# Kernel tuning notes

Measured on AMD Instinct MI355X. Metric: run time of the kernel, lower is better.

## Reference

```python
import jax, jax.numpy as jnp
import numpy as np

N = 512   # state size
D = 512   # input/output feature size
L = 16384 # sequence length


def setup_inputs() -> dict:
    key = jax.random.key(0)
    kA, kB, kC, ku = jax.random.split(key, 4)
    # Scale/shift A so eigenvalues have negative real part (circular law radius 1,
    # shifted by -1.5) -> stable recurrence over L steps; raw randn(N,N) would overflow.
    A = jax.random.normal(kA, (N, N), dtype=jnp.float32) / np.float32(np.sqrt(N)) - 1.5 * jnp.eye(N, dtype=jnp.float32)
    B = jax.random.normal(kB, (N, D), dtype=jnp.float32)
    C = jax.random.normal(kC, (D, N), dtype=jnp.float32)
    u = jax.random.normal(ku, (L, D), dtype=jnp.float32)
    return {"A": A, "B": B, "C": C, "u": u}


def reference(A, B, C, u):
    # run_SSM with discretization='bilinear' (the default)
    Lseq = u.shape[0]
    n = A.shape[0]
    step = 1.0 / Lseq
    I = jnp.eye(n, dtype=A.dtype)
    BL = jnp.linalg.inv(I - A * (step / 2.0))
    Ab = BL @ (I + A * (step / 2.0))          # [N, N]
    Bb = (BL * step) @ B                       # [N, D]  (torch: BL * step @ B)
    # Precompute Bb @ u_k for all k in one GEMM: [L, N]
    Bu = u @ Bb.T

    def step_fn(x, bu_k):
        x = Ab @ x + bu_k                      # x_{k} = Ab x_{k-1} + Bb u_k
        return x, x

    x0 = jnp.zeros((n,), dtype=A.dtype)
    _, xs = jax.lax.scan(step_fn, x0, Bu)      # xs: [L, N]
    ys = xs @ C.T                              # y_k = Cb x_k -> [L, D]
    return ys
```

## Files before the change

kernel.cpp:

```cpp
#include <hip/hip_runtime.h>
#include <hip/hip_bf16.h>

static constexpr int N = 512;
static constexpr int L = 16384;
static constexpr int SQX = 16;

typedef short s16x8 __attribute__((ext_vector_type(8)));
typedef float f32x4 __attribute__((ext_vector_type(4)));
using bf16 = __hip_bfloat16;

#define GPTR(p) ((const __attribute__((address_space(1))) void*)(p))
#define LPTR(p) ((__attribute__((address_space(3))) void*)(p))
__device__ __forceinline__ void gload16(const void* g, void* l) {
    __builtin_amdgcn_global_load_lds(GPTR(g), LPTR(l), 16, 0, 0);
}

__device__ __forceinline__ void split2(float v, ushort& h, ushort& l) {
    bf16 hb = __float2bfloat16(v);
    h = *reinterpret_cast<ushort*>(&hb);
    bf16 lb = __float2bfloat16(v - __bfloat162float(hb));
    l = *reinterpret_cast<ushort*>(&lb);
}
__device__ __forceinline__ ushort f2h(float v) {
    bf16 hb = __float2bfloat16(v);
    return *reinterpret_cast<ushort*>(&hb);
}
__device__ __forceinline__ float us2f(ushort u) {
    return __bfloat162float(*reinterpret_cast<bf16*>(&u));
}


__global__ void k_zeroinit(int* zb) { zb[blockIdx.x * 256 + threadIdx.x] = 0; }

__global__ void k_prep(const float* __restrict__ A, float* __restrict__ M,
                       float* __restrict__ MT, float h) {
    __shared__ float t[32][33];
    int bx = blockIdx.x * 32, by = blockIdx.y * 32;
    int tx = threadIdx.x, ty = threadIdx.y;
#pragma unroll
    for (int j = 0; j < 32; j += 8) {
        float v = A[(by + ty + j) * N + bx + tx] * h;
        t[ty + j][tx] = v;
        M[(by + ty + j) * N + bx + tx] = v;
    }
    __syncthreads();
#pragma unroll
    for (int j = 0; j < 32; j += 8) MT[(bx + ty + j) * N + by + tx] = t[tx][ty + j];
}

__global__ void k_buildDT(const float* __restrict__ M, const float* __restrict__ M2,
                          bf16* __restrict__ Dh, bf16* __restrict__ Dl,
                          float* __restrict__ DTf, bf16* __restrict__ DTh,
                          bf16* __restrict__ DTl, float* __restrict__ BLm) {
    __shared__ float t[32][33];
    int bx = blockIdx.x * 32, by = blockIdx.y * 32;
    int tx = threadIdx.x, ty = threadIdx.y;
#pragma unroll
    for (int j = 0; j < 32; j += 8) {
        int row = by + ty + j, col = bx + tx;
        size_t off = (size_t)row * N + col;
        float m = M[off], m2 = M2[off];
        float d = 2.0f * (m + m2);
        t[ty + j][tx] = d;
        ushort h, l;
        split2(d, h, l);
        *reinterpret_cast<ushort*>(Dh + off) = h;
        *reinterpret_cast<ushort*>(Dl + off) = l;
        BLm[off] = ((row == col) ? 1.0f : 0.0f) + m + m2;
    }
    __syncthreads();
#pragma unroll
    for (int j = 0; j < 32; j += 8) {
        float v = t[tx][ty + j];
        size_t off = (size_t)(bx + ty + j) * N + by + tx;
        DTf[off] = v;
        ushort h, l;
        split2(v, h, l);
        *reinterpret_cast<ushort*>(DTh + off) = h;
        *reinterpret_cast<ushort*>(DTl + off) = l;
    }
}

__global__ void k_split4(const float* __restrict__ in, bf16* __restrict__ hi,
                         bf16* __restrict__ lo, int n4) {
    int i = blockIdx.x * 256 + threadIdx.x;
    if (i >= n4) return;
    float4 v = reinterpret_cast<const float4*>(in)[i];
    ushort ht[4], lt[4];
    split2(v.x, ht[0], lt[0]);
    split2(v.y, ht[1], lt[1]);
    split2(v.z, ht[2], lt[2]);
    split2(v.w, ht[3], lt[3]);
    *reinterpret_cast<ushort4*>(hi + 4 * (size_t)i) = *reinterpret_cast<ushort4*>(ht);
    *reinterpret_cast<ushort4*>(lo + 4 * (size_t)i) = *reinterpret_cast<ushort4*>(lt);
}

__global__ void k_transpose(const float* __restrict__ in, float* __restrict__ out) {
    __shared__ float t[32][33];
    int bx = blockIdx.x * 32, by = blockIdx.y * 32;
    int tx = threadIdx.x, ty = threadIdx.y;
#pragma unroll
    for (int j = 0; j < 32; j += 8) t[ty + j][tx] = in[(by + ty + j) * N + bx + tx];
    __syncthreads();
#pragma unroll
    for (int j = 0; j < 32; j += 8) out[(bx + ty + j) * N + by + tx] = t[tx][ty + j];
}

__global__ __launch_bounds__(256) void k_qsq(
    const float* __restrict__ Asrc, const float* __restrict__ Bmat,
    float* __restrict__ OUT, bf16* __restrict__ Sh, bf16* __restrict__ Sl, float scale) {
    __shared__ float As[32][64];
    __shared__ float Bs[32][64];
    const int tid = threadIdx.x;
    const int brow = blockIdx.x * 64;
    const int bcol = blockIdx.y * 64;
    const int tx = tid & 15, ty = tid >> 4;
    float acc[4][4] = {};

    for (int k0 = 0; k0 < N; k0 += 32) {
#pragma unroll
        for (int q = 0; q < 2; ++q) {
            int idx = tid * 2 + q;
            int row = idx >> 3;
            int kq = (idx & 7) << 2;
            float4 va = *(const float4*)(Asrc + (long)(brow + row) * N + k0 + kq);
            As[kq + 0][row] = va.x; As[kq + 1][row] = va.y;
            As[kq + 2][row] = va.z; As[kq + 3][row] = va.w;
            float4 vb = *(const float4*)(Bmat + (long)(bcol + row) * N + k0 + kq);
            Bs[kq + 0][row] = vb.x; Bs[kq + 1][row] = vb.y;
            Bs[kq + 2][row] = vb.z; Bs[kq + 3][row] = vb.w;
        }
        __syncthreads();
#pragma unroll
        for (int kk = 0; kk < 32; ++kk) {
            float a[4], b[4];
            *(float4*)&a[0] = *(const float4*)&As[kk][ty * 4];
            *(float4*)&b[0] = *(const float4*)&Bs[kk][tx * 4];
#pragma unroll
            for (int i = 0; i < 4; ++i)
#pragma unroll
                for (int j = 0; j < 4; ++j) acc[i][j] = fmaf(a[i], b[j], acc[i][j]);
        }
        __syncthreads();
    }
#pragma unroll
    for (int i = 0; i < 4; ++i) {
        long off = (long)(brow + ty * 4 + i) * N + bcol + tx * 4;
        float4 o = make_float4(acc[i][0] * scale, acc[i][1] * scale,
                               acc[i][2] * scale, acc[i][3] * scale);
        *(float4*)(OUT + off) = o;
        ushort ht[4], lt[4];
        split2(o.x, ht[0], lt[0]); split2(o.y, ht[1], lt[1]);
        split2(o.z, ht[2], lt[2]); split2(o.w, ht[3], lt[3]);
        *reinterpret_cast<ushort4*>(Sh + off) = *reinterpret_cast<ushort4*>(ht);
        *reinterpret_cast<ushort4*>(Sl + off) = *reinterpret_cast<ushort4*>(lt);
    }
}

__global__ __launch_bounds__(256, 3) void k_bu(
    const float* __restrict__ u, const bf16* __restrict__ Bbh,
    bf16* __restrict__ Xoh, bf16* __restrict__ Xol)
{
    __shared__ char smem[32768];
    const int tid = threadIdx.x;
    const int wave = tid >> 6, lane = tid & 63;
    const int wm = wave >> 1, wn = wave & 1;
    const int rl = lane & 15, rh = lane >> 4;
    const long brow = (long)blockIdx.x * 128;
    const int bcol = blockIdx.y * 128;

    f32x4 acc[4][4];
#pragma unroll
    for (int m = 0; m < 4; ++m)
#pragma unroll
        for (int n = 0; n < 4; ++n) acc[m][n] = (f32x4){0.f, 0.f, 0.f, 0.f};

    const float* aptr[2]; int awoff[2];
    const char* pB[2]; int wb[2];
#pragma unroll
    for (int q = 0; q < 2; ++q) {
        int idx = q * 256 + tid;
        int row = idx >> 2, slot = idx & 3;
        int sp = slot ^ ((row >> 1) & 3);
        aptr[q] = u + (brow + row) * N + slot * 8;
        awoff[q] = row * 64 + sp * 16;
        pB[q] = (const char*)(Bbh + (long)(bcol + row) * N + sp * 8);
        wb[q] = (q * 256 + wave * 64) * 16;
    }

    auto stageA = [&](int t, char* buf) {
#pragma unroll
        for (int q = 0; q < 2; ++q) {
            f32x4 v0 = *reinterpret_cast<const f32x4*>(aptr[q] + t * 32);
            f32x4 v1 = *reinterpret_cast<const f32x4*>(aptr[q] + t * 32 + 4);
            s16x8 h;
            h[0] = (short)f2h(v0[0]); h[1] = (short)f2h(v0[1]);
            h[2] = (short)f2h(v0[2]); h[3] = (short)f2h(v0[3]);
            h[4] = (short)f2h(v1[0]); h[5] = (short)f2h(v1[1]);
            h[6] = (short)f2h(v1[2]); h[7] = (short)f2h(v1[3]);
            *reinterpret_cast<s16x8*>(buf + awoff[q]) = h;
        }
    };
    auto stageB = [&](int t, char* buf) {
#pragma unroll
        for (int q = 0; q < 2; ++q) gload16(pB[q] + t * 64, buf + 8192 + wb[q]);
    };

    stageA(0, smem);
    stageB(0, smem);
    __syncthreads();

    for (int t = 0; t < 16; ++t) {
        const char* base = smem + (t & 1) * 16384;
        s16x8 a[4], b[4];
#pragma unroll
        for (int m = 0; m < 4; ++m) {
            int row = wm * 64 + m * 16 + rl;
            a[m] = *reinterpret_cast<const s16x8*>(base + row * 64 + (rh ^ ((row >> 1) & 3)) * 16);
        }
#pragma unroll
        for (int n = 0; n < 4; ++n) {
            int row = wn * 64 + n * 16 + rl;
            b[n] = *reinterpret_cast<const s16x8*>(base + 8192 + row * 64 + (rh ^ ((row >> 1) & 3)) * 16);
        }
        if (t + 1 < 16) {
            char* nb = smem + ((t + 1) & 1) * 16384;
            stageA(t + 1, nb);
            stageB(t + 1, nb);
        }
#pragma unroll
        for (int m = 0; m < 4; ++m)
#pragma unroll
            for (int n = 0; n < 4; ++n)
                acc[m][n] = __builtin_amdgcn_mfma_f32_16x16x32_bf16(a[m], b[n], acc[m][n], 0, 0, 0);
        __syncthreads();
    }

    float* eld = (float*)smem;
    const int erow = tid >> 2;
    const int ec   = (tid & 3) * 8;
    for (int h = 0; h < 2; ++h) {
        if (wm == h) {
#pragma unroll
            for (int m = 0; m < 4; ++m)
#pragma unroll
                for (int q = 0; q < 4; ++q) {
                    int br = m * 16 + rh * 4 + q;
                    int sw = (br & 7) << 2;
#pragma unroll
                    for (int n = 0; n < 4; ++n) {
                        int col = wn * 64 + n * 16 + rl;
                        eld[br * 128 + (col ^ sw)] = acc[m][n][q];
                    }
                }
        }
        __syncthreads();
        {
            long gi = brow + h * 64 + erow;
            const int sw = (erow & 7) << 2;
            long gb = gi * N + bcol;
#pragma unroll
            for (int s = 0; s < 4; ++s) {
                int c = ec + s * 32;
                f32x4 v0 = *reinterpret_cast<const f32x4*>(&eld[erow * 128 + (c ^ sw)]);
                f32x4 v1 = *reinterpret_cast<const f32x4*>(&eld[erow * 128 + ((c ^ sw) ^ 4)]);
                float r[8];
                *reinterpret_cast<f32x4*>(&r[0]) = v0;
                *reinterpret_cast<f32x4*>(&r[4]) = v1;
                ushort oh[8], ol[8];
#pragma unroll
                for (int j = 0; j < 8; ++j) split2(r[j], oh[j], ol[j]);
                *reinterpret_cast<int4*>(Xoh + gb + c) = *reinterpret_cast<int4*>(oh);
                *reinterpret_cast<int4*>(Xol + gb + c) = *reinterpret_cast<int4*>(ol);
            }
        }
        __syncthreads();
    }
}

__global__ __launch_bounds__(256, 3) void k_fin(
    const bf16* __restrict__ Xh, const bf16* __restrict__ Ch, float* __restrict__ Of)
{
    __shared__ char smem[32768];
    const int tid = threadIdx.x;
    const int wave = tid >> 6, lane = tid & 63;
    const int wm = wave >> 1, wn = wave & 1;
    const int rl = lane & 15, rh = lane >> 4;
    const long brow = (long)blockIdx.x * 128;
    const int bcol = blockIdx.y * 128;

    f32x4 acc[4][4];
#pragma unroll
    for (int m = 0; m < 4; ++m)
#pragma unroll
        for (int n = 0; n < 4; ++n) acc[m][n] = (f32x4){0.f, 0.f, 0.f, 0.f};

    const char* pA[2]; const char* pB[2]; int wb[2];
#pragma unroll
    for (int q = 0; q < 2; ++q) {
        int idx = q * 256 + tid;
        int row = idx >> 2, slot = idx & 3;
        int sp = slot ^ ((row >> 1) & 3);
        pA[q] = (const char*)(Xh + (brow + row) * N + sp * 8);
        pB[q] = (const char*)(Ch + (long)(bcol + row) * N + sp * 8);
        wb[q] = (q * 256 + wave * 64) * 16;
    }

#pragma unroll
    for (int q = 0; q < 2; ++q) {
        gload16(pA[q], smem + 0    + wb[q]);
        gload16(pB[q], smem + 8192 + wb[q]);
    }
    __syncthreads();

    for (int t = 0; t < 16; ++t) {
        const char* base = smem + (t & 1) * 16384;
        s16x8 a[4], b[4];
#pragma unroll
        for (int m = 0; m < 4; ++m) {
            int row = wm * 64 + m * 16 + rl;
            a[m] = *reinterpret_cast<const s16x8*>(base + row * 64 + (rh ^ ((row >> 1) & 3)) * 16);
        }
#pragma unroll
        for (int n = 0; n < 4; ++n) {
            int row = wn * 64 + n * 16 + rl;
            b[n] = *reinterpret_cast<const s16x8*>(base + 8192 + row * 64 + (rh ^ ((row >> 1) & 3)) * 16);
        }
        if (t + 1 < 16) {
            const int kb = (t + 1) * 64;
            char* nb = smem + ((t + 1) & 1) * 16384;
#pragma unroll
            for (int q = 0; q < 2; ++q) {
                gload16(pA[q] + kb, nb + 0    + wb[q]);
                gload16(pB[q] + kb, nb + 8192 + wb[q]);
            }
        }
#pragma unroll
        for (int m = 0; m < 4; ++m)
#pragma unroll
            for (int n = 0; n < 4; ++n)
                acc[m][n] = __builtin_amdgcn_mfma_f32_16x16x32_bf16(a[m], b[n], acc[m][n], 0, 0, 0);
        __syncthreads();
    }

    float* eld = (float*)smem;
    const int erow = tid >> 2;
    const int ec   = (tid & 3) * 8;
    for (int h = 0; h < 2; ++h) {
        if (wm == h) {
#pragma unroll
            for (int m = 0; m < 4; ++m)
#pragma unroll
                for (int q = 0; q < 4; ++q) {
                    int br = m * 16 + rh * 4 + q;
                    int sw = (br & 7) << 2;
#pragma unroll
                    for (int n = 0; n < 4; ++n) {
                        int col = wn * 64 + n * 16 + rl;
                        eld[br * 128 + (col ^ sw)] = acc[m][n][q];
                    }
                }
        }
        __syncthreads();
        {
            long gi = brow + h * 64 + erow;
            const int sw = (erow & 7) << 2;
            long gb = gi * N + bcol;
#pragma unroll
            for (int s = 0; s < 4; ++s) {
                int c = ec + s * 32;
                f32x4 v0 = *reinterpret_cast<const f32x4*>(&eld[erow * 128 + (c ^ sw)]);
                f32x4 v1 = *reinterpret_cast<const f32x4*>(&eld[erow * 128 + ((c ^ sw) ^ 4)]);
                *reinterpret_cast<f32x4*>(Of + gb + c)     = v0;
                *reinterpret_cast<f32x4*>(Of + gb + c + 4) = v1;
            }
        }
        __syncthreads();
    }
}

__global__ __launch_bounds__(256, 3) void k_drnd(
    const bf16* __restrict__ Xih, const bf16* __restrict__ Xil,
    bf16* __restrict__ Xoh, bf16* __restrict__ Xol,
    const bf16* __restrict__ Dh, const bf16* __restrict__ Dl,
    const bf16* __restrict__ DTh, const bf16* __restrict__ DTl,
    const float* __restrict__ DTf,
    bf16* __restrict__ Dnh, bf16* __restrict__ Dnl,
    bf16* __restrict__ DTnh, bf16* __restrict__ DTnl, float* __restrict__ DTfn,
    int shift, int doSq, const bf16* __restrict__ zb)
{
    __shared__ char smem[32768];
    const int tid = threadIdx.x;
    const int wave = tid >> 6, lane = tid & 63;
    const int wm = wave >> 1, wn = wave & 1;
    const int rl = lane & 15, rh = lane >> 4;

    if (blockIdx.x < SQX) {
        if (!doSq) return;
        int sidx = (int)blockIdx.x * (int)gridDim.y + (int)blockIdx.y;
        const int ti = (sidx >> 3) * 64, tj = (sidx & 7) * 64;

        f32x4 acc[2][2];
#pragma unroll
        for (int m = 0; m < 2; ++m)
#pragma unroll
            for (int n = 0; n < 2; ++n) acc[m][n] = (f32x4){0.f, 0.f, 0.f, 0.f};

        int row = tid >> 2, slot = tid & 3;
        int sp = slot ^ ((row >> 1) & 3);
        const char* pAh = (const char*)(DTh + (size_t)(ti + row) * N + sp * 8);
        const char* pAl = (const char*)(DTl + (size_t)(ti + row) * N + sp * 8);
        const char* pBh = (const char*)(Dh + (size_t)(tj + row) * N + sp * 8);
        const char* pBl = (const char*)(Dl + (size_t)(tj + row) * N + sp * 8);
        const int wb = wave * 1024;

        gload16(pAh, smem + 0     + wb);
        gload16(pAl, smem + 4096  + wb);
        gload16(pBh, smem + 8192  + wb);
        gload16(pBl, smem + 12288 + wb);
        __syncthreads();

        for (int t = 0; t < 16; ++t) {
            const char* base = smem + (t & 1) * 16384;
            s16x8 ah[2], al[2], bh[2], bl[2];
#pragma unroll
            for (int m = 0; m < 2; ++m) {
                int r2 = wm * 32 + m * 16 + rl;
                int off = r2 * 64 + (rh ^ ((r2 >> 1) & 3)) * 16;
                ah[m] = *reinterpret_cast<const s16x8*>(base + off);
                al[m] = *reinterpret_cast<const s16x8*>(base + 4096 + off);
            }
#pragma unroll
            for (int n = 0; n < 2; ++n) {
                int r2 = wn * 32 + n * 16 + rl;
                int off = r2 * 64 + (rh ^ ((r2 >> 1) & 3)) * 16;
                bh[n] = *reinterpret_cast<const s16x8*>(base + 8192 + off);
                bl[n] = *reinterpret_cast<const s16x8*>(base + 12288 + off);
            }
            if (t + 1 < 16) {
                const int kb = (t + 1) * 64;
                char* nb = smem + ((t + 1) & 1) * 16384;
                gload16(pAh + kb, nb + 0     + wb);
                gload16(pAl + kb, nb + 4096  + wb);
                gload16(pBh + kb, nb + 8192  + wb);
                gload16(pBl + kb, nb + 12288 + wb);
            }
#pragma unroll
            for (int m = 0; m < 2; ++m)
#pragma unroll
                for (int n = 0; n < 2; ++n) {
                    acc[m][n] = __builtin_amdgcn_mfma_f32_16x16x32_bf16(ah[m], bh[n], acc[m][n], 0, 0, 0);
                    acc[m][n] = __builtin_amdgcn_mfma_f32_16x16x32_bf16(ah[m], bl[n], acc[m][n], 0, 0, 0);
                    acc[m][n] = __builtin_amdgcn_mfma_f32_16x16x32_bf16(al[m], bh[n], acc[m][n], 0, 0, 0);
                }
            __syncthreads();
        }

#pragma unroll
        for (int m = 0; m < 2; ++m)
#pragma unroll
            for (int n = 0; n < 2; ++n)
#pragma unroll
                for (int q = 0; q < 4; ++q) {
                    int i = ti + wm * 32 + m * 16 + rh * 4 + q;
                    int j = tj + wn * 32 + n * 16 + rl;
                    size_t off = (size_t)i * N + j;
                    float v = acc[m][n][q] + 2.0f * DTf[off];
                    DTfn[off] = v;
                    ushort h, l;
                    split2(v, h, l);
                    *reinterpret_cast<ushort*>(DTnh + off) = h;
                    *reinterpret_cast<ushort*>(DTnl + off) = l;
                    size_t offT = (size_t)j * N + i;
                    *reinterpret_cast<ushort*>(Dnh + offT) = h;
                    *reinterpret_cast<ushort*>(Dnl + offT) = l;
                }
        return;
    }

    int bigbx = (int)blockIdx.x - SQX;
    const int sb = shift >> 7;
    int rowBlk = bigbx + sb;
    bool isCopy = false;
    if (rowBlk >= (L / 128)) { rowBlk -= (L / 128); isCopy = true; }
    const long brow = (long)rowBlk * 128;
    const int bcol = blockIdx.y * 128;

    if (isCopy) {
#pragma unroll
        for (int j = 0; j < 8; ++j) {
            int c = j * 256 + tid;
            long off = (brow + (c >> 4)) * N + bcol + (c & 15) * 8;
            *reinterpret_cast<int4*>(Xoh + off) = *reinterpret_cast<const int4*>(Xih + off);
            *reinterpret_cast<int4*>(Xol + off) = *reinterpret_cast<const int4*>(Xil + off);
        }
        return;
    }

    f32x4 acc[4][4];
#pragma unroll
    for (int m = 0; m < 4; ++m)
#pragma unroll
        for (int n = 0; n < 4; ++n) acc[m][n] = (f32x4){0.f, 0.f, 0.f, 0.f};

    const char* pA[2]; const char* pB[2]; int wb[2];
#pragma unroll
    for (int q = 0; q < 2; ++q) {
        int idx = q * 256 + tid;
        int row = idx >> 2, slot = idx & 3;
        int sp = slot ^ ((row >> 1) & 3);
        long gra = brow + row - (long)shift;
        pA[q] = (gra >= 0) ? (const char*)(Xih + gra * N + sp * 8)
                           : (const char*)(zb + sp * 8);
        pB[q] = (const char*)(Dh + (long)(bcol + row) * N + sp * 8);
        wb[q] = (q * 256 + wave * 64) * 16;
    }

#pragma unroll
    for (int q = 0; q < 2; ++q) {
        gload16(pA[q], smem + 0    + wb[q]);
        gload16(pB[q], smem + 8192 + wb[q]);
    }
    __syncthreads();

    for (int t = 0; t < 16; ++t) {
        const char* base = smem + (t & 1) * 16384;
        s16x8 a[4], b[4];
#pragma unroll
        for (int m = 0; m < 4; ++m) {
            int row = wm * 64 + m * 16 + rl;
            a[m] = *reinterpret_cast<const s16x8*>(base + row * 64 + (rh ^ ((row >> 1) & 3)) * 16);
        }
#pragma unroll
        for (int n = 0; n < 4; ++n) {
            int row = wn * 64 + n * 16 + rl;
            b[n] = *reinterpret_cast<const s16x8*>(base + 8192 + row * 64 + (rh ^ ((row >> 1) & 3)) * 16);
        }
        if (t + 1 < 16) {
            const int kb = (t + 1) * 64;
            char* nb = smem + ((t + 1) & 1) * 16384;
#pragma unroll
            for (int q = 0; q < 2; ++q) {
                gload16(pA[q] + kb, nb + 0    + wb[q]);
                gload16(pB[q] + kb, nb + 8192 + wb[q]);
            }
        }
#pragma unroll
        for (int m = 0; m < 4; ++m)
#pragma unroll
            for (int n = 0; n < 4; ++n)
                acc[m][n] = __builtin_amdgcn_mfma_f32_16x16x32_bf16(a[m], b[n], acc[m][n], 0, 0, 0);
        __syncthreads();
    }

    float* eld = (float*)smem;
    const int erow = tid >> 2;
    const int ec   = (tid & 3) * 8;
    for (int h = 0; h < 2; ++h) {
        if (wm == h) {
#pragma unroll
            for (int m = 0; m < 4; ++m)
#pragma unroll
                for (int q = 0; q < 4; ++q) {
                    int br = m * 16 + rh * 4 + q;
                    int sw = (br & 7) << 2;
#pragma unroll
                    for (int n = 0; n < 4; ++n) {
                        int col = wn * 64 + n * 16 + rl;
                        eld[br * 128 + (col ^ sw)] = acc[m][n][q];
                    }
                }
        }
        __syncthreads();
        {
            long gi = brow + h * 64 + erow;
            bool hasS = gi >= (long)shift;
            const int sw = (erow & 7) << 2;
            long gb = gi * N + bcol;
            long gs = gb - (long)shift * N;
#pragma unroll
            for (int s = 0; s < 4; ++s) {
                int c = ec + s * 32;
                f32x4 v0 = *reinterpret_cast<const f32x4*>(&eld[erow * 128 + (c ^ sw)]);
                f32x4 v1 = *reinterpret_cast<const f32x4*>(&eld[erow * 128 + ((c ^ sw) ^ 4)]);
                float r[8];
                *reinterpret_cast<f32x4*>(&r[0]) = v0;
                *reinterpret_cast<f32x4*>(&r[4]) = v1;
                ushort vh[8], vl[8];
                *reinterpret_cast<int4*>(vh) = *reinterpret_cast<const int4*>(Xih + gb + c);
                *reinterpret_cast<int4*>(vl) = *reinterpret_cast<const int4*>(Xil + gb + c);
#pragma unroll
                for (int j = 0; j < 8; ++j) r[j] += us2f(vh[j]) + us2f(vl[j]);
                if (hasS) {
                    *reinterpret_cast<int4*>(vh) = *reinterpret_cast<const int4*>(Xih + gs + c);
                    *reinterpret_cast<int4*>(vl) = *reinterpret_cast<const int4*>(Xil + gs + c);
#pragma unroll
                    for (int j = 0; j < 8; ++j) r[j] += us2f(vh[j]) + us2f(vl[j]);
                }
                ushort oh[8], ol[8];
#pragma unroll
                for (int j = 0; j < 8; ++j) split2(r[j], oh[j], ol[j]);
                *reinterpret_cast<int4*>(Xoh + gb + c) = *reinterpret_cast<int4*>(oh);
                *reinterpret_cast<int4*>(Xol + gb + c) = *reinterpret_cast<int4*>(ol);
            }
        }
        __syncthreads();
    }
}


extern "C" void kernel_launch(void* const* d_in, const int* in_sizes, int n_in,
                              void* d_out, int out_size, void* d_ws, size_t ws_size,
                              hipStream_t stream) {
    (void)in_sizes; (void)n_in; (void)out_size; (void)ws_size;
    const float* A = (const float*)d_in[0];
    const float* B = (const float*)d_in[1];
    const float* C = (const float*)d_in[2];
    const float* u = (const float*)d_in[3];

    const size_t NN = (size_t)N * N;
    const size_t LN = (size_t)L * N;

    bf16* X1h = (bf16*)d_out;
    bf16* X1l = X1h + LN;

    char* w = (char*)d_ws;
    bf16* X0h = (bf16*)w;      w += LN * 2;
    bf16* X0l = (bf16*)w;      w += LN * 2;
    bf16 *Dh_[2], *Dl_[2], *DTh_[2], *DTl_[2];
    float* DTf_[2];
    for (int s = 0; s < 2; ++s) {
        Dh_[s]  = (bf16*)w;    w += NN * 2;
        Dl_[s]  = (bf16*)w;    w += NN * 2;
        DTh_[s] = (bf16*)w;    w += NN * 2;
        DTl_[s] = (bf16*)w;    w += NN * 2;
        DTf_[s] = (float*)w;   w += NN * 4;
    }
    float* M   = (float*)w;    w += NN * 4;
    float* MT  = (float*)w;    w += NN * 4;
    float* M2  = (float*)w;    w += NN * 4;
    float* BLm = (float*)w;    w += NN * 4;
    float* BT  = (float*)w;    w += NN * 4;
    float* Bbf = (float*)w;    w += NN * 4;
    bf16* Bbh  = (bf16*)w;     w += NN * 2;
    bf16* Bbl  = (bf16*)w;     w += NN * 2;
    bf16* Ch   = (bf16*)w;     w += NN * 2;
    bf16* Cl   = (bf16*)w;     w += NN * 2;
    bf16* zb   = (bf16*)w;     w += 2048;

    const float step = 1.0f / (float)L;

    dim3 b256(256);
    dim3 bT(32, 8), gT(N / 32, N / 32);
    dim3 g64(N / 64, N / 64);
    dim3 gBig(L / 128, N / 128);
    dim3 gRound(SQX + L / 128, N / 128);
    dim3 gS4n((int)(NN / 4 / 256));

    k_zeroinit<<<2, 256, 0, stream>>>((int*)zb);

    k_prep<<<gT, bT, 0, stream>>>(A, M, MT, step * 0.5f);
    k_qsq<<<g64, b256, 0, stream>>>(M, MT, M2, Bbh, Bbl, 1.0f);
    k_buildDT<<<gT, bT, 0, stream>>>(M, M2, Dh_[0], Dl_[0],
                                     DTf_[0], DTh_[0], DTl_[0], BLm);
    k_transpose<<<gT, bT, 0, stream>>>(B, BT);
    k_qsq<<<g64, b256, 0, stream>>>(BLm, BT, Bbf, Bbh, Bbl, step);
    k_split4<<<gS4n, b256, 0, stream>>>(C, Ch, Cl, (int)(NN / 4));

    k_bu<<<gBig, b256, 0, stream>>>(u, Bbh, X0h, X0l);

    for (int r = 0; r < 14; ++r) {
        int s = r & 1, nx = s ^ 1;
        bf16* Xih = (r & 1) ? X1h : X0h;  bf16* Xil = (r & 1) ? X1l : X0l;
        bf16* Xoh = (r & 1) ? X0h : X1h;  bf16* Xol = (r & 1) ? X0l : X1l;
        int doSq = (r < 13) ? 1 : 0;
        k_drnd<<<gRound, b256, 0, stream>>>(
            Xih, Xil, Xoh, Xol, Dh_[s], Dl_[s],
            DTh_[s], DTl_[s], DTf_[s],
            Dh_[nx], Dl_[nx], DTh_[nx], DTl_[nx], DTf_[nx], 1 << r, doSq, zb);
    }

    k_fin<<<gBig, b256, 0, stream>>>(X0h, Ch, (float*)d_out);
}
```

Before: 473.0 us.

## Fold first and last doubling rounds into the input and output GEMMs

The first doubling round is absorbed into the Bu GEMM: it now also multiplies u shifted by one row against a precomputed second input matrix, which needs extra setup kernels (k_qsqadd, k_dsq). The last round is absorbed into the output GEMM: the second half of the rows adds a second product using a modified C matrix. This removes two full L×N×N scan-round launches. In exchange the Bu and output GEMMs do about twice the MFMA work, use 64 KB of LDS with lower occupancy, and add some small setup matmuls.

```diff
diff --git a/kernel.cpp b/kernel.cpp
--- a/kernel.cpp
+++ b/kernel.cpp
@@ -50,6 +50,7 @@
 
 __global__ void k_buildDT(const float* __restrict__ M, const float* __restrict__ M2,
                           bf16* __restrict__ Dh, bf16* __restrict__ Dl,
+                          float* __restrict__ D0f,
                           float* __restrict__ DTf, bf16* __restrict__ DTh,
                           bf16* __restrict__ DTl, float* __restrict__ BLm) {
     __shared__ float t[32][33];
@@ -62,6 +63,7 @@
         float m = M[off], m2 = M2[off];
         float d = 2.0f * (m + m2);
         t[ty + j][tx] = d;
+        D0f[off] = d;
         ushort h, l;
         split2(d, h, l);
         *reinterpret_cast<ushort*>(Dh + off) = h;
@@ -157,15 +159,157 @@
     }
 }
 
-__global__ __launch_bounds__(256, 3) void k_bu(
-    const float* __restrict__ u, const bf16* __restrict__ Bbh,
-    bf16* __restrict__ Xoh, bf16* __restrict__ Xol)
+__global__ __launch_bounds__(256) void k_qsqadd(
+    const float* __restrict__ Asrc, const float* __restrict__ Bmat,
+    const float* __restrict__ Cadd, bf16* __restrict__ Sh, bf16* __restrict__ Sl) {
+    __shared__ float As[32][64];
+    __shared__ float Bs[32][64];
+    const int tid = threadIdx.x;
+    const int brow = blockIdx.x * 64;
+    const int bcol = blockIdx.y * 64;
+    const int tx = tid & 15, ty = tid >> 4;
+    float acc[4][4] = {};
+
+    for (int k0 = 0; k0 < N; k0 += 32) {
+#pragma unroll
+        for (int q = 0; q < 2; ++q) {
+            int idx = tid * 2 + q;
+            int row = idx >> 3;
+            int kq = (idx & 7) << 2;
+            float4 va = *(const float4*)(Asrc + (long)(brow + row) * N + k0 + kq);
+            As[kq + 0][row] = va.x; As[kq + 1][row] = va.y;
+            As[kq + 2][row] = va.z; As[kq + 3][row] = va.w;
+            float4 vb = *(const float4*)(Bmat + (long)(bcol + row) * N + k0 + kq);
+            Bs[kq + 0][row] = vb.x; Bs[kq + 1][row] = vb.y;
+            Bs[kq + 2][row] = vb.z; Bs[kq + 3][row] = vb.w;
+        }
+        __syncthreads();
+#pragma unroll
+        for (int kk = 0; kk < 32; ++kk) {
+            float a[4], b[4];
+            *(float4*)&a[0] = *(const float4*)&As[kk][ty * 4];
+            *(float4*)&b[0] = *(const float4*)&Bs[kk][tx * 4];
+#pragma unroll
+            for (int i = 0; i < 4; ++i)
+#pragma unroll
+                for (int j = 0; j < 4; ++j) acc[i][j] = fmaf(a[i], b[j], acc[i][j]);
+        }
+        __syncthreads();
+    }
+#pragma unroll
+    for (int i = 0; i < 4; ++i) {
+        long off = (long)(brow + ty * 4 + i) * N + bcol + tx * 4;
+        float4 cv = *(const float4*)(Cadd + off);
+        float r0 = cv.x + acc[i][0], r1 = cv.y + acc[i][1];
+        float r2 = cv.z + acc[i][2], r3 = cv.w + acc[i][3];
+        ushort ht[4], lt[4];
+        split2(r0, ht[0], lt[0]); split2(r1, ht[1], lt[1]);
+        split2(r2, ht[2], lt[2]); split2(r3, ht[3], lt[3]);
+        *reinterpret_cast<ushort4*>(Sh + off) = *reinterpret_cast<ushort4*>(ht);
+        *reinterpret_cast<ushort4*>(Sl + off) = *reinterpret_cast<ushort4*>(lt);
+    }
+}
+
+__global__ __launch_bounds__(256) void k_dsq(
+    const bf16* __restrict__ Dh, const bf16* __restrict__ Dl,
+    const bf16* __restrict__ DTh, const bf16* __restrict__ DTl,
+    const float* __restrict__ DTf,
+    bf16* __restrict__ Dnh, bf16* __restrict__ Dnl,
+    bf16* __restrict__ DTnh, bf16* __restrict__ DTnl, float* __restrict__ DTfn)
 {
     __shared__ char smem[32768];
     const int tid = threadIdx.x;
     const int wave = tid >> 6, lane = tid & 63;
     const int wm = wave >> 1, wn = wave & 1;
     const int rl = lane & 15, rh = lane >> 4;
+    const int ti = blockIdx.x * 64, tj = blockIdx.y * 64;
+
+    f32x4 acc[2][2];
+#pragma unroll
+    for (int m = 0; m < 2; ++m)
+#pragma unroll
+        for (int n = 0; n < 2; ++n) acc[m][n] = (f32x4){0.f, 0.f, 0.f, 0.f};
+
+    int row = tid >> 2, slot = tid & 3;
+    int sp = slot ^ ((row >> 1) & 3);
+    const char* pAh = (const char*)(DTh + (size_t)(ti + row) * N + sp * 8);
+    const char* pAl = (const char*)(DTl + (size_t)(ti + row) * N + sp * 8);
+    const char* pBh = (const char*)(Dh + (size_t)(tj + row) * N + sp * 8);
+    const char* pBl = (const char*)(Dl + (size_t)(tj + row) * N + sp * 8);
+    const int wb = wave * 1024;
+
+    gload16(pAh, smem + 0     + wb);
+    gload16(pAl, smem + 4096  + wb);
+    gload16(pBh, smem + 8192  + wb);
+    gload16(pBl, smem + 12288 + wb);
+    __syncthreads();
+
+    for (int t = 0; t < 16; ++t) {
+        const char* base = smem + (t & 1) * 16384;
+        s16x8 ah[2], al[2], bh[2], bl[2];
+#pragma unroll
+        for (int m = 0; m < 2; ++m) {
+            int r2 = wm * 32 + m * 16 + rl;
+            int off = r2 * 64 + (rh ^ ((r2 >> 1) & 3)) * 16;
+            ah[m] = *reinterpret_cast<const s16x8*>(base + off);
+            al[m] = *reinterpret_cast<const s16x8*>(base + 4096 + off);
+        }
+#pragma unroll
+        for (int n = 0; n < 2; ++n) {
+            int r2 = wn * 32 + n * 16 + rl;
+            int off = r2 * 64 + (rh ^ ((r2 >> 1) & 3)) * 16;
+            bh[n] = *reinterpret_cast<const s16x8*>(base + 8192 + off);
+            bl[n] = *reinterpret_cast<const s16x8*>(base + 12288 + off);
+        }
+        if (t + 1 < 16) {
+            const int kb = (t + 1) * 64;
+            char* nb = smem + ((t + 1) & 1) * 16384;
+            gload16(pAh + kb, nb + 0     + wb);
+            gload16(pAl + kb, nb + 4096  + wb);
+            gload16(pBh + kb, nb + 8192  + wb);
+            gload16(pBl + kb, nb + 12288 + wb);
+        }
+#pragma unroll
+        for (int m = 0; m < 2; ++m)
+#pragma unroll
+            for (int n = 0; n < 2; ++n) {
+                acc[m][n] = __builtin_amdgcn_mfma_f32_16x16x32_bf16(ah[m], bh[n], acc[m][n], 0, 0, 0);
+                acc[m][n] = __builtin_amdgcn_mfma_f32_16x16x32_bf16(ah[m], bl[n], acc[m][n], 0, 0, 0);
+                acc[m][n] = __builtin_amdgcn_mfma_f32_16x16x32_bf16(al[m], bh[n], acc[m][n], 0, 0, 0);
+            }
+        __syncthreads();
+    }
+
+#pragma unroll
+    for (int m = 0; m < 2; ++m)
+#pragma unroll
+        for (int n = 0; n < 2; ++n)
+#pragma unroll
+            for (int q = 0; q < 4; ++q) {
+                int i = ti + wm * 32 + m * 16 + rh * 4 + q;
+                int j = tj + wn * 32 + n * 16 + rl;
+                size_t off = (size_t)i * N + j;
+                float v = acc[m][n][q] + 2.0f * DTf[off];
+                DTfn[off] = v;
+                ushort h, l;
+                split2(v, h, l);
+                *reinterpret_cast<ushort*>(DTnh + off) = h;
+                *reinterpret_cast<ushort*>(DTnl + off) = l;
+                size_t offT = (size_t)j * N + i;
+                *reinterpret_cast<ushort*>(Dnh + offT) = h;
+                *reinterpret_cast<ushort*>(Dnl + offT) = l;
+            }
+}
+
+__global__ __launch_bounds__(256, 2) void k_bu2(
+    const float* __restrict__ u, const bf16* __restrict__ Bbh,
+    const bf16* __restrict__ Bb2h, bf16* __restrict__ Xoh, bf16* __restrict__ Xol)
+{
+    __shared__ char smem[65536];
+    const int tid = threadIdx.x;
+    const int wave = tid >> 6, lane = tid & 63;
+    const int wm = wave >> 1, wn = wave & 1;
+    const int rl = lane & 15, rh = lane >> 4;
     const long brow = (long)blockIdx.x * 128;
     const int bcol = blockIdx.y * 128;
 
@@ -175,16 +319,20 @@
 #pragma unroll
         for (int n = 0; n < 4; ++n) acc[m][n] = (f32x4){0.f, 0.f, 0.f, 0.f};
 
-    const float* aptr[2]; int awoff[2];
-    const char* pB[2]; int wb[2];
+    const float* aptr[2]; const float* a2ptr[2]; bool a2v[2]; int awoff[2];
+    const char* pB[2]; const char* pB2[2]; int wb[2];
 #pragma unroll
     for (int q = 0; q < 2; ++q) {
         int idx = q * 256 + tid;
         int row = idx >> 2, slot = idx & 3;
         int sp = slot ^ ((row >> 1) & 3);
         aptr[q] = u + (brow + row) * N + slot * 8;
+        long r2 = brow + row - 1;
+        a2v[q] = (r2 >= 0);
+        a2ptr[q] = u + (a2v[q] ? r2 : 0) * N + slot * 8;
         awoff[q] = row * 64 + sp * 16;
-        pB[q] = (const char*)(Bbh + (long)(bcol + row) * N + sp * 8);
+        pB[q]  = (const char*)(Bbh  + (long)(bcol + row) * N + sp * 8);
+        pB2[q] = (const char*)(Bb2h + (long)(bcol + row) * N + sp * 8);
         wb[q] = (q * 256 + wave * 64) * 16;
     }
 
@@ -199,11 +347,24 @@
             h[4] = (short)f2h(v1[0]); h[5] = (short)f2h(v1[1]);
             h[6] = (short)f2h(v1[2]); h[7] = (short)f2h(v1[3]);
             *reinterpret_cast<s16x8*>(buf + awoff[q]) = h;
+            s16x8 h2 = {0, 0, 0, 0, 0, 0, 0, 0};
+            if (a2v[q]) {
+                f32x4 w0 = *reinterpret_cast<const f32x4*>(a2ptr[q] + t * 32);
+                f32x4 w1 = *reinterpret_cast<const f32x4*>(a2ptr[q] + t * 32 + 4);
+                h2[0] = (short)f2h(w0[0]); h2[1] = (short)f2h(w0[1]);
+                h2[2] = (short)f2h(w0[2]); h2[3] = (short)f2h(w0[3]);
+                h2[4] = (short)f2h(w1[0]); h2[5] = (short)f2h(w1[1]);
+                h2[6] = (short)f2h(w1[2]); h2[7] = (short)f2h(w1[3]);
+            }
+            *reinterpret_cast<s16x8*>(buf + 8192 + awoff[q]) = h2;
         }
     };
     auto stageB = [&](int t, char* buf) {
 #pragma unroll
-        for (int q = 0; q < 2; ++q) gload16(pB[q] + t * 64, buf + 8192 + wb[q]);
+        for (int q = 0; q < 2; ++q) {
+            gload16(pB[q]  + t * 64, buf + 16384 + wb[q]);
+            gload16(pB2[q] + t * 64, buf + 24576 + wb[q]);
+        }
     };
 
     stageA(0, smem);
@@ -211,28 +372,34 @@
     __syncthreads();
 
     for (int t = 0; t < 16; ++t) {
-        const char* base = smem + (t & 1) * 16384;
-        s16x8 a[4], b[4];
+        const char* base = smem + (t & 1) * 32768;
+        s16x8 a[4], a2[4], b[4], b2[4];
 #pragma unroll
         for (int m = 0; m < 4; ++m) {
             int row = wm * 64 + m * 16 + rl;
-            a[m] = *reinterpret_cast<const s16x8*>(base + row * 64 + (rh ^ ((row >> 1) & 3)) * 16);
+            int off = row * 64 + (rh ^ ((row >> 1) & 3)) * 16;
+            a[m]  = *reinterpret_cast<const s16x8*>(base + off);
+            a2[m] = *reinterpret_cast<const s16x8*>(base + 8192 + off);
         }
 #pragma unroll
         for (int n = 0; n < 4; ++n) {
             int row = wn * 64 + n * 16 + rl;
-            b[n] = *reinterpret_cast<const s16x8*>(base + 8192 + row * 64 + (rh ^ ((row >> 1) & 3)) * 16);
+            int off = row * 64 + (rh ^ ((row >> 1) & 3)) * 16;
+            b[n]  = *reinterpret_cast<const s16x8*>(base + 16384 + off);
+            b2[n] = *reinterpret_cast<const s16x8*>(base + 24576 + off);
         }
         if (t + 1 < 16) {
-            char* nb = smem + ((t + 1) & 1) * 16384;
+            char* nb = smem + ((t + 1) & 1) * 32768;
             stageA(t + 1, nb);
             stageB(t + 1, nb);
         }
 #pragma unroll
         for (int m = 0; m < 4; ++m)
 #pragma unroll
-            for (int n = 0; n < 4; ++n)
-                acc[m][n] = __builtin_amdgcn_mfma_f32_16x16x32_bf16(a[m], b[n], acc[m][n], 0, 0, 0);
+            for (int n = 0; n < 4; ++n) {
+                acc[m][n] = __builtin_amdgcn_mfma_f32_16x16x32_bf16(a[m],  b[n],  acc[m][n], 0, 0, 0);
+                acc[m][n] = __builtin_amdgcn_mfma_f32_16x16x32_bf16(a2[m], b2[n], acc[m][n], 0, 0, 0);
+            }
         __syncthreads();
     }
 
@@ -278,16 +445,18 @@
     }
 }
 
-__global__ __launch_bounds__(256, 3) void k_fin(
-    const bf16* __restrict__ Xh, const bf16* __restrict__ Ch, float* __restrict__ Of)
+__global__ __launch_bounds__(256, 2) void k_fin2(
+    const bf16* __restrict__ Xh, const bf16* __restrict__ Ch,
+    const bf16* __restrict__ C2h, float* __restrict__ Of)
 {
-    __shared__ char smem[32768];
+    __shared__ char smem[65536];
     const int tid = threadIdx.x;
     const int wave = tid >> 6, lane = tid & 63;
     const int wm = wave >> 1, wn = wave & 1;
     const int rl = lane & 15, rh = lane >> 4;
     const long brow = (long)blockIdx.x * 128;
     const int bcol = blockIdx.y * 128;
+    const bool dual = (brow >= (L / 2));
 
     f32x4 acc[4][4];
 #pragma unroll
@@ -295,26 +464,38 @@
 #pragma unroll
         for (int n = 0; n < 4; ++n) acc[m][n] = (f32x4){0.f, 0.f, 0.f, 0.f};
 
-    const char* pA[2]; const char* pB[2]; int wb[2];
+    const char* pA[2]; const char* pA2[2]; const char* pB[2]; const char* pB2[2];
+    int wb[2];
 #pragma unroll
     for (int q = 0; q < 2; ++q) {
         int idx = q * 256 + tid;
         int row = idx >> 2, slot = idx & 3;
         int sp = slot ^ ((row >> 1) & 3);
-        pA[q] = (const char*)(Xh + (brow + row) * N + sp * 8);
-        pB[q] = (const char*)(Ch + (long)(bcol + row) * N + sp * 8);
+        pA[q]  = (const char*)(Xh + (brow + row) * N + sp * 8);
+        pA2[q] = (const char*)(Xh + (brow + row - (long)(L / 2)) * N + sp * 8);
+        pB[q]  = (const char*)(Ch  + (long)(bcol + row) * N + sp * 8);
+        pB2[q] = (const char*)(C2h + (long)(bcol + row) * N + sp * 8);
         wb[q] = (q * 256 + wave * 64) * 16;
     }
 
-#pragma unroll
-    for (int q = 0; q < 2; ++q) {
-        gload16(pA[q], smem + 0    + wb[q]);
-        gload16(pB[q], smem + 8192 + wb[q]);
-    }
+    auto stage = [&](int t, char* buf) {
+        const int kb = t * 64;
+#pragma unroll
+        for (int q = 0; q < 2; ++q) {
+            gload16(pA[q] + kb, buf + wb[q]);
+            gload16(pB[q] + kb, buf + 16384 + wb[q]);
+            if (dual) {
+                gload16(pA2[q] + kb, buf + 8192 + wb[q]);
+                gload16(pB2[q] + kb, buf + 24576 + wb[q]);
+            }
+        }
+    };
+
+    stage(0, smem);
     __syncthreads();
 
     for (int t = 0; t < 16; ++t) {
-        const char* base = smem + (t & 1) * 16384;
+        const char* base = smem + (t & 1) * 32768;
         s16x8 a[4], b[4];
 #pragma unroll
         for (int m = 0; m < 4; ++m) {
@@ -324,22 +505,34 @@
 #pragma unroll
         for (int n = 0; n < 4; ++n) {
             int row = wn * 64 + n * 16 + rl;
-            b[n] = *reinterpret_cast<const s16x8*>(base + 8192 + row * 64 + (rh ^ ((row >> 1) & 3)) * 16);
-        }
-        if (t + 1 < 16) {
-            const int kb = (t + 1) * 64;
-            char* nb = smem + ((t + 1) & 1) * 16384;
-#pragma unroll
-            for (int q = 0; q < 2; ++q) {
-                gload16(pA[q] + kb, nb + 0    + wb[q]);
-                gload16(pB[q] + kb, nb + 8192 + wb[q]);
-            }
-        }
+            b[n] = *reinterpret_cast<const s16x8*>(base + 16384 + row * 64 + (rh ^ ((row >> 1) & 3)) * 16);
+        }
+        s16x8 a2[4], b2[4];
+        if (dual) {
+#pragma unroll
+            for (int m = 0; m < 4; ++m) {
+                int row = wm * 64 + m * 16 + rl;
+                a2[m] = *reinterpret_cast<const s16x8*>(base + 8192 + row * 64 + (rh ^ ((row >> 1) & 3)) * 16);
+            }
+#pragma unroll
+            for (int n = 0; n < 4; ++n) {
+                int row = wn * 64 + n * 16 + rl;
+                b2[n] = *reinterpret_cast<const s16x8*>(base + 24576 + row * 64 + (rh ^ ((row >> 1) & 3)) * 16);
+            }
+        }
+        if (t + 1 < 16) stage(t + 1, smem + ((t + 1) & 1) * 32768);
 #pragma unroll
         for (int m = 0; m < 4; ++m)
 #pragma unroll
             for (int n = 0; n < 4; ++n)
                 acc[m][n] = __builtin_amdgcn_mfma_f32_16x16x32_bf16(a[m], b[n], acc[m][n], 0, 0, 0);
+        if (dual) {
+#pragma unroll
+            for (int m = 0; m < 4; ++m)
+#pragma unroll
+                for (int n = 0; n < 4; ++n)
+                    acc[m][n] = __builtin_amdgcn_mfma_f32_16x16x32_bf16(a2[m], b2[n], acc[m][n], 0, 0, 0);
+        }
         __syncthreads();
     }
 
@@ -636,17 +829,23 @@
         DTl_[s] = (bf16*)w;    w += NN * 2;
         DTf_[s] = (float*)w;   w += NN * 4;
     }
-    float* M   = (float*)w;    w += NN * 4;
-    float* MT  = (float*)w;    w += NN * 4;
-    float* M2  = (float*)w;    w += NN * 4;
-    float* BLm = (float*)w;    w += NN * 4;
-    float* BT  = (float*)w;    w += NN * 4;
-    float* Bbf = (float*)w;    w += NN * 4;
-    bf16* Bbh  = (bf16*)w;     w += NN * 2;
-    bf16* Bbl  = (bf16*)w;     w += NN * 2;
-    bf16* Ch   = (bf16*)w;     w += NN * 2;
-    bf16* Cl   = (bf16*)w;     w += NN * 2;
-    bf16* zb   = (bf16*)w;     w += 2048;
+    float* M    = (float*)w;   w += NN * 4;
+    float* MT   = (float*)w;   w += NN * 4;
+    float* M2   = (float*)w;   w += NN * 4;
+    float* BLm  = (float*)w;   w += NN * 4;
+    float* BT   = (float*)w;   w += NN * 4;
+    float* Bbf  = (float*)w;   w += NN * 4;
+    float* D0f  = (float*)w;   w += NN * 4;
+    float* BbT  = (float*)w;   w += NN * 4;
+    bf16* Bbh   = (bf16*)w;    w += NN * 2;
+    bf16* Bbl   = (bf16*)w;    w += NN * 2;
+    bf16* Bb2h  = (bf16*)w;    w += NN * 2;
+    bf16* Bb2l  = (bf16*)w;    w += NN * 2;
+    bf16* Ch    = (bf16*)w;    w += NN * 2;
+    bf16* Cl    = (bf16*)w;    w += NN * 2;
+    bf16* C2h   = (bf16*)w;    w += NN * 2;
+    bf16* C2l   = (bf16*)w;    w += NN * 2;
+    bf16* zb    = (bf16*)w;    w += 2048;
 
     const float step = 1.0f / (float)L;
 
@@ -661,24 +860,29 @@
 
     k_prep<<<gT, bT, 0, stream>>>(A, M, MT, step * 0.5f);
     k_qsq<<<g64, b256, 0, stream>>>(M, MT, M2, Bbh, Bbl, 1.0f);
-    k_buildDT<<<gT, bT, 0, stream>>>(M, M2, Dh_[0], Dl_[0],
+    k_buildDT<<<gT, bT, 0, stream>>>(M, M2, Dh_[0], Dl_[0], D0f,
                                      DTf_[0], DTh_[0], DTl_[0], BLm);
     k_transpose<<<gT, bT, 0, stream>>>(B, BT);
     k_qsq<<<g64, b256, 0, stream>>>(BLm, BT, Bbf, Bbh, Bbl, step);
+    k_transpose<<<gT, bT, 0, stream>>>(Bbf, BbT);
+    k_qsqadd<<<g64, b256, 0, stream>>>(D0f, BbT, Bbf, Bb2h, Bb2l);
+    k_dsq<<<g64, b256, 0, stream>>>(Dh_[0], Dl_[0], DTh_[0], DTl_[0], DTf_[0],
+                                    Dh_[1], Dl_[1], DTh_[1], DTl_[1], DTf_[1]);
     k_split4<<<gS4n, b256, 0, stream>>>(C, Ch, Cl, (int)(NN / 4));
 
-    k_bu<<<gBig, b256, 0, stream>>>(u, Bbh, X0h, X0l);
-
-    for (int r = 0; r < 14; ++r) {
+    k_bu2<<<gBig, b256, 0, stream>>>(u, Bbh, Bb2h, X0h, X0l);
+
+    for (int r = 1; r <= 12; ++r) {
         int s = r & 1, nx = s ^ 1;
-        bf16* Xih = (r & 1) ? X1h : X0h;  bf16* Xil = (r & 1) ? X1l : X0l;
-        bf16* Xoh = (r & 1) ? X0h : X1h;  bf16* Xol = (r & 1) ? X0l : X1l;
-        int doSq = (r < 13) ? 1 : 0;
+        bf16* Xih = (r & 1) ? X0h : X1h;  bf16* Xil = (r & 1) ? X0l : X1l;
+        bf16* Xoh = (r & 1) ? X1h : X0h;  bf16* Xol = (r & 1) ? X1l : X0l;
         k_drnd<<<gRound, b256, 0, stream>>>(
             Xih, Xil, Xoh, Xol, Dh_[s], Dl_[s],
             DTh_[s], DTl_[s], DTf_[s],
-            Dh_[nx], Dl_[nx], DTh_[nx], DTl_[nx], DTf_[nx], 1 << r, doSq, zb);
-    }
-
-    k_fin<<<gBig, b256, 0, stream>>>(X0h, Ch, (float*)d_out);
-}
+            Dh_[nx], Dl_[nx], DTh_[nx], DTl_[nx], DTf_[nx], 1 << r, 1, zb);
+    }
+
+    k_qsqadd<<<g64, b256, 0, stream>>>(C, DTf_[1], C, C2h, C2l);
+
+    k_fin2<<<gBig, b256, 0, stream>>>(X0h, Ch, C2h, (float*)d_out);
+}
```

New measurement: 504.0 us. 6.6% more time.
